# Kernel tuning notes

Measured on AMD Instinct MI355X. Metric: run time of the kernel, lower is better.

## Reference

```python
import jax, jax.numpy as jnp
import numpy as np

N_NEURONS = 100000
NNZ = 3200000
N_SENSORY = 5000
BATCH = 16
NUM_LAYERS = 8
THRESHOLD = 0.01
TANH_STEEPNESS = 5.0


def setup_inputs() -> dict:
    key = jax.random.key(0)
    k1, k2, k3, k4 = jax.random.split(key, 4)
    inputs = jax.random.uniform(k1, (BATCH, N_SENSORY, NUM_LAYERS), dtype=jnp.float32)
    # sparse connectome in COO form; small values so activations stay in a sane range
    weight_vals = jax.random.normal(k2, (NNZ,), dtype=jnp.float32) * 0.1
    weight_rows = jax.random.randint(k3, (NNZ,), 0, N_NEURONS, dtype=jnp.int32)
    weight_cols = jax.random.randint(k4, (NNZ,), 0, N_NEURONS, dtype=jnp.int32)
    sensory_indices = jnp.arange(N_SENSORY, dtype=jnp.int32)
    return {
        "inputs": inputs,
        "weight_vals": weight_vals,
        "weight_rows": weight_rows,
        "weight_cols": weight_cols,
        "sensory_indices": sensory_indices,
    }


def _spmm(vals, rows, cols, x):
    # x: (N, B); y[r, b] = sum_{e: rows[e]==r} vals[e] * x[cols[e], b]
    return jax.ops.segment_sum(vals[:, None] * x[cols], rows, num_segments=N_NEURONS)


def _activate(y):
    y = jnp.where(y >= THRESHOLD, y, jnp.zeros_like(y))
    return jnp.tanh(TANH_STEEPNESS * y)


def reference(inputs, weight_vals, weight_rows, weight_cols, sensory_indices):
    B, S, T = inputs.shape  # T == num_layers
    # preprocess sensory input: threshold then clamp to <= 1
    inp = jnp.where(inputs >= THRESHOLD, inputs, jnp.zeros_like(inputs))
    inp = jnp.minimum(inp, jnp.ones_like(inp))
    # state x: (N, B)
    full_input = jnp.zeros((N_NEURONS, B), inputs.dtype).at[sensory_indices].add(inp[:, :, 0].T)
    x = _activate(_spmm(weight_vals, weight_rows, weight_cols, full_input))
    acts = []
    for layer in range(1, T):
        # inject sensory input for this time step and clamp to <= 1
        x = x.at[sensory_indices].add(inp[:, :, layer].T)
        x = jnp.minimum(x, jnp.ones_like(x))
        acts.append(x)
        x = _activate(_spmm(weight_vals, weight_rows, weight_cols, x))
    acts.append(x)  # last layer: no injection
    # (T, N, B) -> (B, N, T), matching torch vmap'd cat along time dim
    return jnp.stack(acts, axis=0).transpose(2, 1, 0)
```

## Files before the change

### kernel.cpp

```cpp
#include <hip/hip_runtime.h>


#define N_NEURONS 100000
#define NNZ_CNT   3200000
#define N_SENSORY 5000
#define BATCH     16
#define T_LAYERS  8
#define THRESH    0.01f
#define STEEP     5.0f

#define NB (N_NEURONS * BATCH)
#define NT (N_NEURONS * T_LAYERS)
#define ST (N_SENSORY * T_LAYERS)

#define FXSCALE   17592186044416.0f
#define FXINV     (1.0 / 17592186044416.0)

#define LBITS   9
#define BROWS   (1 << LBITS)
#define NBUCKET ((N_NEURONS + BROWS - 1) / BROWS)
#define EPB     8192
#define NBLK_A  ((NNZ_CNT + EPB - 1) / EPB)

__device__ __forceinline__ float thresh_clamp_inp(float u) {
    u = (u >= THRESH) ? u : 0.0f;
    return fminf(u, 1.0f);
}
__device__ __forceinline__ float activate(float y) {
    y = (y >= THRESH) ? y : 0.0f;
    return tanhf(STEEP * y);
}


__global__ void k_init(const float* __restrict__ inp, float* __restrict__ state0,
                       int* __restrict__ btotal) {
    int stride = gridDim.x * blockDim.x;
    for (int i = blockIdx.x * blockDim.x + threadIdx.x; i < NB; i += stride) {
        int n = i >> 4, b = i & 15;
        float v = 0.0f;
        if (n < N_SENSORY) v = thresh_clamp_inp(inp[b * ST + n * T_LAYERS + 0]);
        state0[i] = v;
        if (i < NBUCKET) btotal[i] = 0;
    }
}

__global__ void __launch_bounds__(1024) k_bcount(const int* __restrict__ rows,
                                                 int* __restrict__ btotal) {
    __shared__ int cnt[NBUCKET];
    const int e0 = blockIdx.x * EPB;
    for (int i = threadIdx.x; i < NBUCKET; i += 1024) cnt[i] = 0;
    __syncthreads();
    #pragma unroll
    for (int i = 0; i < EPB / 1024; ++i) {
        int e = e0 + i * 1024 + threadIdx.x;
        if (e < NNZ_CNT) atomicAdd(&cnt[rows[e] >> LBITS], 1);
    }
    __syncthreads();
    for (int i = threadIdx.x; i < NBUCKET; i += 1024)
        if (cnt[i]) atomicAdd(&btotal[i], cnt[i]);
}

__global__ void k_bscan(const int* __restrict__ btotal, int* __restrict__ bbase,
                        int* __restrict__ bcur, int* __restrict__ row_ptr) {
    __shared__ int lds[256];
    int tid = threadIdx.x;
    int v = (tid < NBUCKET) ? btotal[tid] : 0;
    lds[tid] = v;
    __syncthreads();
    for (int off = 1; off < 256; off <<= 1) {
        int add = (tid >= off) ? lds[tid - off] : 0;
        __syncthreads();
        lds[tid] += add;
        __syncthreads();
    }
    if (tid < NBUCKET) {
        bbase[tid] = lds[tid] - v;
        bcur[tid]  = lds[tid] - v;
    }
    if (tid == 0) { bbase[NBUCKET] = NNZ_CNT; row_ptr[N_NEURONS] = NNZ_CNT; }
}

__global__ void __launch_bounds__(1024) k_passA(const float* __restrict__ vals,
                                                const int* __restrict__ rows,
                                                const int* __restrict__ cols,
                                                int* bcur,
                                                int2* __restrict__ packed_tmp) {
    __shared__ int cnt[NBUCKET];
    __shared__ int base[NBUCKET];
    const int e0 = blockIdx.x * EPB;
    for (int i = threadIdx.x; i < NBUCKET; i += 1024) cnt[i] = 0;
    __syncthreads();
    #pragma unroll
    for (int i = 0; i < EPB / 1024; ++i) {
        int e = e0 + i * 1024 + threadIdx.x;
        if (e < NNZ_CNT) atomicAdd(&cnt[rows[e] >> LBITS], 1);
    }
    __syncthreads();
    for (int i = threadIdx.x; i < NBUCKET; i += 1024) {
        int c = cnt[i];
        base[i] = (c > 0) ? atomicAdd(&bcur[i], c) : 0;
        cnt[i] = 0;
    }
    __syncthreads();
    #pragma unroll
    for (int i = 0; i < EPB / 1024; ++i) {
        int e = e0 + i * 1024 + threadIdx.x;
        if (e < NNZ_CNT) {
            int r = rows[e];
            int k = r >> LBITS;
            int pos = base[k] + atomicAdd(&cnt[k], 1);
            packed_tmp[pos] = make_int2((cols[e] << LBITS) | (r & (BROWS - 1)),
                                        __float_as_int(vals[e]));
        }
    }
}

__global__ void __launch_bounds__(1024) k_passB(const int* __restrict__ bbase,
                                                const int2* __restrict__ packed_tmp,
                                                int2* __restrict__ packed,
                                                int* __restrict__ row_ptr) {
    __shared__ int cnt[BROWS];
    __shared__ int scn[BROWS];
    const int tid = threadIdx.x;
    const int k  = blockIdx.x;
    const int r0 = k * BROWS;
    const int nr = min(BROWS, N_NEURONS - r0);
    const int P0 = bbase[k], P1 = bbase[k + 1];
    for (int i = tid; i < BROWS; i += 1024) cnt[i] = 0;
    __syncthreads();
    for (int i = P0 + tid; i < P1; i += 1024)
        atomicAdd(&cnt[packed_tmp[i].x & (BROWS - 1)], 1);
    __syncthreads();
    if (tid < BROWS) scn[tid] = cnt[tid];
    __syncthreads();
    for (int off = 1; off < BROWS; off <<= 1) {
        int add = (tid < BROWS && tid >= off) ? scn[tid - off] : 0;
        __syncthreads();
        if (tid < BROWS) scn[tid] += add;
        __syncthreads();
    }
    if (tid < BROWS) {
        int ex = P0 + scn[tid] - cnt[tid];
        if (tid < nr) row_ptr[r0 + tid] = ex;
        scn[tid] = ex;
    }
    __syncthreads();
    for (int i = P0 + tid; i < P1; i += 1024) {
        int2 pe = packed_tmp[i];
        int d = atomicAdd(&scn[pe.x & (BROWS - 1)], 1);
        packed[d] = make_int2(pe.x >> LBITS, pe.y);
    }
}

__global__ void __launch_bounds__(256) k_layer(const int* __restrict__ row_ptr,
                                               const int2* __restrict__ packed,
                                               const float* __restrict__ state_in,
                                               const float* __restrict__ inp,
                                               float* __restrict__ plane_out,
                                               int t) {
    int tid = blockIdx.x * blockDim.x + threadIdx.x;
    int r = tid >> 4, b = tid & 15;
    if (r >= N_NEURONS) return;
    int s = row_ptr[r], e = row_ptr[r + 1];
    long long acc = 0;
    for (int base = s; base < e; base += 16) {
        int idx = base + b;
        int2 pe = (idx < e) ? packed[idx] : make_int2(0, 0);
        #pragma unroll
        for (int j = 0; j < 16; ++j) {
            int   c = __shfl(pe.x, j, 16);
            float v = __int_as_float(__shfl(pe.y, j, 16));
            float xv = state_in[c * BATCH + b];
            acc += (long long)llrintf(v * xv * FXSCALE);
        }
    }
    float y = (float)((double)acc * FXINV);
    float a = activate(y);
    if (t < T_LAYERS - 1) {
        if (r < N_SENSORY) a += thresh_clamp_inp(inp[b * ST + r * T_LAYERS + (t + 1)]);
        a = fminf(a, 1.0f);
    }
    plane_out[r * BATCH + b] = a;
}

__global__ void k_out(const float* __restrict__ planes, float* __restrict__ out) {
    int i = blockIdx.x * blockDim.x + threadIdx.x;
    if (i >= NB) return;
    int n = i >> 4, b = i & 15;
    float4 o0, o1;
    o0.x = planes[0 * NB + i]; o0.y = planes[1 * NB + i];
    o0.z = planes[2 * NB + i]; o0.w = planes[3 * NB + i];
    o1.x = planes[4 * NB + i]; o1.y = planes[5 * NB + i];
    o1.z = planes[6 * NB + i]; o1.w = planes[7 * NB + i];
    float4* dst = (float4*)&out[b * NT + n * T_LAYERS];
    dst[0] = o0; dst[1] = o1;
}

__global__ void k2_init(const float* __restrict__ inp, float* __restrict__ state,
                        long long* __restrict__ acc) {
    int stride = gridDim.x * blockDim.x;
    for (int i = blockIdx.x * blockDim.x + threadIdx.x; i < NB; i += stride) {
        int n = i >> 4, b = i & 15;
        float v = 0.0f;
        if (n < N_SENSORY) v = thresh_clamp_inp(inp[b * ST + n * T_LAYERS + 0]);
        state[i] = v;
        acc[i]   = 0LL;
    }
}
__global__ void __launch_bounds__(256) k2_spmm(const float* __restrict__ vals,
                                               const int* __restrict__ rows,
                                               const int* __restrict__ cols,
                                               const float* __restrict__ state,
                                               long long* acc) {
    int tid = blockIdx.x * blockDim.x + threadIdx.x;
    int b = tid & 15;
    int e = tid >> 4;
    int estride = (gridDim.x * blockDim.x) >> 4;
    for (; e < NNZ_CNT; e += estride) {
        int   c  = cols[e];
        float xv = state[c * BATCH + b];
        float v  = vals[e];
        long long fx = llrintf(v * xv * FXSCALE);
        if (fx != 0LL) {
            int r = rows[e];
            atomicAdd((unsigned long long*)&acc[r * BATCH + b], (unsigned long long)fx);
        }
    }
}
__global__ void k2_act_inject(long long* acc, const float* __restrict__ inp,
                              float* __restrict__ state, float* __restrict__ out, int t) {
    int stride = gridDim.x * blockDim.x;
    for (int i = blockIdx.x * blockDim.x + threadIdx.x; i < NB; i += stride) {
        int n = i >> 4, b = i & 15;
        float y = (float)((double)acc[i] * FXINV);
        acc[i] = 0LL;
        float v = activate(y);
        if (n < N_SENSORY) v += thresh_clamp_inp(inp[b * ST + n * T_LAYERS + (t + 1)]);
        v = fminf(v, 1.0f);
        state[i] = v;
        out[b * NT + n * T_LAYERS + t] = v;
    }
}
__global__ void k2_act_final(const long long* __restrict__ acc, float* __restrict__ out) {
    int stride = gridDim.x * blockDim.x;
    for (int i = blockIdx.x * blockDim.x + threadIdx.x; i < NB; i += stride) {
        int n = i >> 4, b = i & 15;
        float y = (float)((double)acc[i] * FXINV);
        out[b * NT + n * T_LAYERS + (T_LAYERS - 1)] = activate(y);
    }
}

extern "C" void kernel_launch(void* const* d_in, const int* in_sizes, int n_in,
                              void* d_out, int out_size, void* d_ws, size_t ws_size,
                              hipStream_t stream) {
    const float* inputs = (const float*)d_in[0];
    const float* vals   = (const float*)d_in[1];
    const int*   rows   = (const int*)  d_in[2];
    const int*   cols   = (const int*)  d_in[3];
    float* out = (float*)d_out;

    const size_t sz_planes = (size_t)T_LAYERS * NB * 4;
    const size_t sz_packed = (size_t)NNZ_CNT * 8;
    const size_t sz_rowptr = ((size_t)N_NEURONS + 2) * 4;
    const size_t sz_btotal = (size_t)(NBUCKET + 8) * 4;
    const size_t sz_bbase  = (size_t)(NBUCKET + 8) * 4;
    const size_t sz_bcur   = (size_t)(NBUCKET + 8) * 4;
    const size_t REQ = sz_planes + sz_packed + sz_rowptr + sz_btotal + sz_bbase + sz_bcur;

    const int block = 256;

    if (ws_size >= REQ) {
        char* ws = (char*)d_ws;
        float* planes  = (float*)ws;
        int2*  packed  = (int2*)(ws + sz_planes);
        int*   row_ptr = (int*)(ws + sz_planes + sz_packed);
        int*   btotal  = (int*)(ws + sz_planes + sz_packed + sz_rowptr);
        int*   bbase   = (int*)(ws + sz_planes + sz_packed + sz_rowptr + sz_btotal);
        int*   bcur    = (int*)(ws + sz_planes + sz_packed + sz_rowptr + sz_btotal + sz_bbase);
        float* state0  = planes + (size_t)(T_LAYERS - 1) * NB;
        int2*  packed_tmp = (int2*)planes;

        const int grid_nb = (NB + block - 1) / block;

        k_init<<<grid_nb, block, 0, stream>>>(inputs, state0, btotal);
        k_bcount<<<NBLK_A, 1024, 0, stream>>>(rows, btotal);
        k_bscan<<<1, 256, 0, stream>>>(btotal, bbase, bcur, row_ptr);
        k_passA<<<NBLK_A, 1024, 0, stream>>>(vals, rows, cols, bcur, packed_tmp);
        k_passB<<<NBUCKET, 1024, 0, stream>>>(bbase, packed_tmp, packed, row_ptr);

        for (int t = 0; t < T_LAYERS; ++t) {
            const float* sin_ = (t == 0) ? state0 : planes + (size_t)(t - 1) * NB;
            k_layer<<<grid_nb, block, 0, stream>>>(row_ptr, packed, sin_, inputs,
                                                   planes + (size_t)t * NB, t);
        }
        k_out<<<grid_nb, block, 0, stream>>>(planes, out);
    } else {
        long long* acc   = (long long*)d_ws;
        float*     state = (float*)(acc + NB);
        const int grid_ew = 2048, grid_sp = 2048;
        k2_init<<<grid_ew, block, 0, stream>>>(inputs, state, acc);
        for (int t = 0; t < T_LAYERS; ++t) {
            k2_spmm<<<grid_sp, block, 0, stream>>>(vals, rows, cols, state, acc);
            if (t < T_LAYERS - 1)
                k2_act_inject<<<grid_ew, block, 0, stream>>>(acc, inputs, state, out, t);
            else
                k2_act_final<<<grid_ew, block, 0, stream>>>(acc, out);
        }
    }
}
```

Measured before the change: 426.6 us.

## Rebuild CSR conversion as deterministic chunked counting sort with float accumulation

Replaces the atomic-cursor two-pass bucket sort with a deterministic counting sort. Per-chunk histograms are followed by column scans, and placement uses wave-level ballot match to aggregate LDS atomics, applied to both the bucket and row passes. The SpMV layer kernel switches from 64-bit fixed-point accumulation with llrintf to plain fmaf float accumulation, relying on the deterministic ordering for reproducibility. This adds more kernel launches and scratch matrices, and float accumulation can change rounding compared with the exact fixed-point sum.

Result: slower. 439.0 us (+2.9%).

```diff
diff --git a/kernel.cpp b/kernel.cpp
--- a/kernel.cpp
+++ b/kernel.cpp
@@ -13,14 +13,16 @@
 #define NT (N_NEURONS * T_LAYERS)
 #define ST (N_SENSORY * T_LAYERS)
 
+#define LBITS    9
+#define BROWS    (1 << LBITS)
+#define NBUCKET  ((N_NEURONS + BROWS - 1) / BROWS)
+#define EPC      512
+#define NCHUNK_A (NNZ_CNT / EPC)
+#define MAXW     34
+#define NCHUNK_B (NBUCKET * MAXW)
+
 #define FXSCALE   17592186044416.0f
 #define FXINV     (1.0 / 17592186044416.0)
-
-#define LBITS   9
-#define BROWS   (1 << LBITS)
-#define NBUCKET ((N_NEURONS + BROWS - 1) / BROWS)
-#define EPB     8192
-#define NBLK_A  ((NNZ_CNT + EPB - 1) / EPB)
 
 __device__ __forceinline__ float thresh_clamp_inp(float u) {
     u = (u >= THRESH) ? u : 0.0f;
@@ -32,36 +34,50 @@
 }
 
 
-__global__ void k_init(const float* __restrict__ inp, float* __restrict__ state0,
-                       int* __restrict__ btotal) {
-    int stride = gridDim.x * blockDim.x;
-    for (int i = blockIdx.x * blockDim.x + threadIdx.x; i < NB; i += stride) {
-        int n = i >> 4, b = i & 15;
-        float v = 0.0f;
-        if (n < N_SENSORY) v = thresh_clamp_inp(inp[b * ST + n * T_LAYERS + 0]);
-        state0[i] = v;
-        if (i < NBUCKET) btotal[i] = 0;
-    }
-}
-
-__global__ void __launch_bounds__(1024) k_bcount(const int* __restrict__ rows,
-                                                 int* __restrict__ btotal) {
-    __shared__ int cnt[NBUCKET];
-    const int e0 = blockIdx.x * EPB;
-    for (int i = threadIdx.x; i < NBUCKET; i += 1024) cnt[i] = 0;
-    __syncthreads();
-    #pragma unroll
-    for (int i = 0; i < EPB / 1024; ++i) {
-        int e = e0 + i * 1024 + threadIdx.x;
-        if (e < NNZ_CNT) atomicAdd(&cnt[rows[e] >> LBITS], 1);
-    }
-    __syncthreads();
-    for (int i = threadIdx.x; i < NBUCKET; i += 1024)
-        if (cnt[i]) atomicAdd(&btotal[i], cnt[i]);
+__global__ void __launch_bounds__(256) k_countA(const int* __restrict__ rows,
+                                                int* __restrict__ M) {
+    __shared__ int cnt[4][NBUCKET];
+    int wv = threadIdx.x >> 6, ln = threadIdx.x & 63;
+    int chunk = blockIdx.x * 4 + wv;
+    for (int j = ln; j < NBUCKET; j += 64) cnt[wv][j] = 0;
+    __syncthreads();
+    if (chunk < NCHUNK_A) {
+        int base = chunk * EPC;
+        #pragma unroll
+        for (int it = 0; it < 8; ++it)
+            atomicAdd(&cnt[wv][rows[base + it * 64 + ln] >> LBITS], 1);
+    }
+    __syncthreads();
+    if (chunk < NCHUNK_A)
+        for (int j = ln; j < NBUCKET; j += 64) M[chunk * NBUCKET + j] = cnt[wv][j];
+}
+
+__global__ void __launch_bounds__(1024) k_scanA(int* __restrict__ M,
+                                                int* __restrict__ btotal) {
+    __shared__ int lds[1024];
+    int j = blockIdx.x, tid = threadIdx.x;
+    int running = 0;
+    for (int c0 = 0; c0 < NCHUNK_A; c0 += 1024) {
+        int c = c0 + tid;
+        int v = (c < NCHUNK_A) ? M[c * NBUCKET + j] : 0;
+        lds[tid] = v;
+        __syncthreads();
+        for (int off = 1; off < 1024; off <<= 1) {
+            int add = (tid >= off) ? lds[tid - off] : 0;
+            __syncthreads();
+            lds[tid] += add;
+            __syncthreads();
+        }
+        if (c < NCHUNK_A) M[c * NBUCKET + j] = running + lds[tid] - v;
+        int total = lds[1023];
+        __syncthreads();
+        running += total;
+    }
+    if (tid == 0) btotal[j] = running;
 }
 
 __global__ void k_bscan(const int* __restrict__ btotal, int* __restrict__ bbase,
-                        int* __restrict__ bcur, int* __restrict__ row_ptr) {
+                        int* __restrict__ row_ptr) {
     __shared__ int lds[256];
     int tid = threadIdx.x;
     int v = (tid < NBUCKET) ? btotal[tid] : 0;
@@ -73,83 +89,146 @@
         lds[tid] += add;
         __syncthreads();
     }
-    if (tid < NBUCKET) {
-        bbase[tid] = lds[tid] - v;
-        bcur[tid]  = lds[tid] - v;
-    }
+    if (tid < NBUCKET) bbase[tid] = lds[tid] - v;
     if (tid == 0) { bbase[NBUCKET] = NNZ_CNT; row_ptr[N_NEURONS] = NNZ_CNT; }
 }
 
-__global__ void __launch_bounds__(1024) k_passA(const float* __restrict__ vals,
-                                                const int* __restrict__ rows,
+__global__ void __launch_bounds__(256) k_placeA(const int* __restrict__ rows,
                                                 const int* __restrict__ cols,
-                                                int* bcur,
-                                                int2* __restrict__ packed_tmp) {
-    __shared__ int cnt[NBUCKET];
-    __shared__ int base[NBUCKET];
-    const int e0 = blockIdx.x * EPB;
-    for (int i = threadIdx.x; i < NBUCKET; i += 1024) cnt[i] = 0;
-    __syncthreads();
-    #pragma unroll
-    for (int i = 0; i < EPB / 1024; ++i) {
-        int e = e0 + i * 1024 + threadIdx.x;
-        if (e < NNZ_CNT) atomicAdd(&cnt[rows[e] >> LBITS], 1);
-    }
-    __syncthreads();
-    for (int i = threadIdx.x; i < NBUCKET; i += 1024) {
-        int c = cnt[i];
-        base[i] = (c > 0) ? atomicAdd(&bcur[i], c) : 0;
-        cnt[i] = 0;
-    }
-    __syncthreads();
-    #pragma unroll
-    for (int i = 0; i < EPB / 1024; ++i) {
-        int e = e0 + i * 1024 + threadIdx.x;
-        if (e < NNZ_CNT) {
+                                                const float* __restrict__ vals,
+                                                const int* __restrict__ M,
+                                                const int* __restrict__ bbase,
+                                                int2* __restrict__ slab) {
+    __shared__ int cur[4][NBUCKET];
+    int wv = threadIdx.x >> 6, ln = threadIdx.x & 63;
+    int chunk = blockIdx.x * 4 + wv;
+    bool cv = chunk < NCHUNK_A;
+    if (cv)
+        for (int j = ln; j < NBUCKET; j += 64)
+            cur[wv][j] = bbase[j] + M[chunk * NBUCKET + j];
+    __syncthreads();
+    if (cv) {
+        int base = chunk * EPC;
+        #pragma unroll
+        for (int it = 0; it < 8; ++it) {
+            int e = base + it * 64 + ln;
             int r = rows[e];
-            int k = r >> LBITS;
-            int pos = base[k] + atomicAdd(&cnt[k], 1);
-            packed_tmp[pos] = make_int2((cols[e] << LBITS) | (r & (BROWS - 1)),
-                                        __float_as_int(vals[e]));
-        }
-    }
-}
-
-__global__ void __launch_bounds__(1024) k_passB(const int* __restrict__ bbase,
-                                                const int2* __restrict__ packed_tmp,
-                                                int2* __restrict__ packed,
-                                                int* __restrict__ row_ptr) {
+            int key = r >> LBITS;
+            unsigned long long mask = ~0ull;
+            #pragma unroll
+            for (int bit = 0; bit < 8; ++bit) {
+                unsigned long long bb = __ballot((key >> bit) & 1);
+                mask &= ((key >> bit) & 1) ? bb : ~bb;
+            }
+            int rank = __popcll(mask & ((1ull << ln) - 1ull));
+            int cnt  = __popcll(mask);
+            int leader = __ffsll((unsigned long long)mask) - 1;
+            int bpos = 0;
+            if (rank == 0) bpos = atomicAdd(&cur[wv][key], cnt);
+            bpos = __shfl(bpos, leader, 64);
+            slab[bpos + rank] = make_int2((cols[e] << LBITS) | (r & (BROWS - 1)),
+                                          __float_as_int(vals[e]));
+        }
+    }
+}
+
+__global__ void __launch_bounds__(256) k_countB(const int* __restrict__ bbase,
+                                                const int2* __restrict__ slab,
+                                                int* __restrict__ C2) {
     __shared__ int cnt[BROWS];
+    int j = blockIdx.x / MAXW, w = blockIdx.x % MAXW;
+    int P0 = bbase[j], P1 = bbase[j + 1];
+    int s0 = P0 + w * EPC;
+    for (int lr = threadIdx.x; lr < BROWS; lr += 256) cnt[lr] = 0;
+    __syncthreads();
+    if (s0 < P1) {
+        int send = min(s0 + EPC, P1);
+        for (int s = s0 + threadIdx.x; s < send; s += 256)
+            atomicAdd(&cnt[slab[s].x & (BROWS - 1)], 1);
+    }
+    __syncthreads();
+    for (int lr = threadIdx.x; lr < BROWS; lr += 256)
+        C2[blockIdx.x * BROWS + lr] = cnt[lr];
+}
+
+__global__ void __launch_bounds__(512) k_scanB(const int* __restrict__ bbase,
+                                               int* __restrict__ C2,
+                                               int* __restrict__ row_ptr) {
     __shared__ int scn[BROWS];
-    const int tid = threadIdx.x;
-    const int k  = blockIdx.x;
-    const int r0 = k * BROWS;
-    const int nr = min(BROWS, N_NEURONS - r0);
-    const int P0 = bbase[k], P1 = bbase[k + 1];
-    for (int i = tid; i < BROWS; i += 1024) cnt[i] = 0;
-    __syncthreads();
-    for (int i = P0 + tid; i < P1; i += 1024)
-        atomicAdd(&cnt[packed_tmp[i].x & (BROWS - 1)], 1);
-    __syncthreads();
-    if (tid < BROWS) scn[tid] = cnt[tid];
+    int j = blockIdx.x, lr = threadIdx.x;
+    int P0 = bbase[j];
+    int t = 0;
+    for (int w = 0; w < MAXW; ++w) t += C2[(j * MAXW + w) * BROWS + lr];
+    scn[lr] = t;
     __syncthreads();
     for (int off = 1; off < BROWS; off <<= 1) {
-        int add = (tid < BROWS && tid >= off) ? scn[tid - off] : 0;
-        __syncthreads();
-        if (tid < BROWS) scn[tid] += add;
-        __syncthreads();
-    }
-    if (tid < BROWS) {
-        int ex = P0 + scn[tid] - cnt[tid];
-        if (tid < nr) row_ptr[r0 + tid] = ex;
-        scn[tid] = ex;
-    }
-    __syncthreads();
-    for (int i = P0 + tid; i < P1; i += 1024) {
-        int2 pe = packed_tmp[i];
-        int d = atomicAdd(&scn[pe.x & (BROWS - 1)], 1);
-        packed[d] = make_int2(pe.x >> LBITS, pe.y);
-    }
+        int add = (lr >= off) ? scn[lr - off] : 0;
+        __syncthreads();
+        scn[lr] += add;
+        __syncthreads();
+    }
+    int rowbase = P0 + scn[lr] - t;
+    int r = j * BROWS + lr;
+    if (r < N_NEURONS) row_ptr[r] = rowbase;
+    int runw = rowbase;
+    for (int w = 0; w < MAXW; ++w) {
+        int idx = (j * MAXW + w) * BROWS + lr;
+        int c = C2[idx];
+        C2[idx] = runw;
+        runw += c;
+    }
+}
+
+__global__ void __launch_bounds__(256) k_placeB(const int* __restrict__ bbase,
+                                                const int2* __restrict__ slab,
+                                                const int* __restrict__ C2,
+                                                int2* __restrict__ packed) {
+    __shared__ int cur[4][BROWS];
+    int wv = threadIdx.x >> 6, ln = threadIdx.x & 63;
+    int g = blockIdx.x * 4 + wv;
+    bool gv = g < NCHUNK_B;
+    int j = gv ? g / MAXW : 0, w = gv ? g % MAXW : 0;
+    int P0 = bbase[j], P1 = bbase[j + 1];
+    int s0 = P0 + w * EPC;
+    gv = gv && (s0 < P1);
+    if (gv)
+        for (int lr = ln; lr < BROWS; lr += 64) cur[wv][lr] = C2[g * BROWS + lr];
+    __syncthreads();
+    if (gv) {
+        int send = min(s0 + EPC, P1);
+        #pragma unroll
+        for (int it = 0; it < 8; ++it) {
+            int s = s0 + it * 64 + ln;
+            bool act = s < send;
+            unsigned long long amask = __ballot(act);
+            if (act) {
+                int2 pe = slab[s];
+                int key = pe.x & (BROWS - 1);
+                unsigned long long mask = amask;
+                #pragma unroll
+                for (int bit = 0; bit < LBITS; ++bit) {
+                    unsigned long long bb = __ballot((key >> bit) & 1);
+                    mask &= ((key >> bit) & 1) ? bb : ~bb;
+                }
+                int rank = __popcll(mask & ((1ull << ln) - 1ull));
+                int cnt  = __popcll(mask);
+                int leader = __ffsll((unsigned long long)mask) - 1;
+                int bpos = 0;
+                if (rank == 0) bpos = atomicAdd(&cur[wv][key], cnt);
+                bpos = __shfl(bpos, leader, 64);
+                packed[bpos + rank] = make_int2(pe.x >> LBITS, pe.y);
+            }
+        }
+    }
+}
+
+__global__ void k_init(const float* __restrict__ inp, float* __restrict__ state0) {
+    int i = blockIdx.x * blockDim.x + threadIdx.x;
+    if (i >= NB) return;
+    int n = i >> 4, b = i & 15;
+    float v = 0.0f;
+    if (n < N_SENSORY) v = thresh_clamp_inp(inp[b * ST + n * T_LAYERS + 0]);
+    state0[i] = v;
 }
 
 __global__ void __launch_bounds__(256) k_layer(const int* __restrict__ row_ptr,
@@ -162,20 +241,18 @@
     int r = tid >> 4, b = tid & 15;
     if (r >= N_NEURONS) return;
     int s = row_ptr[r], e = row_ptr[r + 1];
-    long long acc = 0;
+    float acc = 0.0f;
     for (int base = s; base < e; base += 16) {
         int idx = base + b;
         int2 pe = (idx < e) ? packed[idx] : make_int2(0, 0);
         #pragma unroll
-        for (int j = 0; j < 16; ++j) {
-            int   c = __shfl(pe.x, j, 16);
-            float v = __int_as_float(__shfl(pe.y, j, 16));
-            float xv = state_in[c * BATCH + b];
-            acc += (long long)llrintf(v * xv * FXSCALE);
-        }
-    }
-    float y = (float)((double)acc * FXINV);
-    float a = activate(y);
+        for (int jj = 0; jj < 16; ++jj) {
+            int   c = __shfl(pe.x, jj, 16);
+            float v = __int_as_float(__shfl(pe.y, jj, 16));
+            acc = fmaf(v, state_in[c * BATCH + b], acc);
+        }
+    }
+    float a = activate(acc);
     if (t < T_LAYERS - 1) {
         if (r < N_SENSORY) a += thresh_clamp_inp(inp[b * ST + r * T_LAYERS + (t + 1)]);
         a = fminf(a, 1.0f);
@@ -217,14 +294,10 @@
     int e = tid >> 4;
     int estride = (gridDim.x * blockDim.x) >> 4;
     for (; e < NNZ_CNT; e += estride) {
-        int   c  = cols[e];
-        float xv = state[c * BATCH + b];
-        float v  = vals[e];
-        long long fx = llrintf(v * xv * FXSCALE);
-        if (fx != 0LL) {
-            int r = rows[e];
-            atomicAdd((unsigned long long*)&acc[r * BATCH + b], (unsigned long long)fx);
-        }
+        float xv = state[cols[e] * BATCH + b];
+        long long fx = llrintf(vals[e] * xv * FXSCALE);
+        if (fx != 0LL)
+            atomicAdd((unsigned long long*)&acc[rows[e] * BATCH + b], (unsigned long long)fx);
     }
 }
 __global__ void k2_act_inject(long long* acc, const float* __restrict__ inp,
@@ -262,10 +335,8 @@
     const size_t sz_planes = (size_t)T_LAYERS * NB * 4;
     const size_t sz_packed = (size_t)NNZ_CNT * 8;
     const size_t sz_rowptr = ((size_t)N_NEURONS + 2) * 4;
-    const size_t sz_btotal = (size_t)(NBUCKET + 8) * 4;
-    const size_t sz_bbase  = (size_t)(NBUCKET + 8) * 4;
-    const size_t sz_bcur   = (size_t)(NBUCKET + 8) * 4;
-    const size_t REQ = sz_planes + sz_packed + sz_rowptr + sz_btotal + sz_bbase + sz_bcur;
+    const size_t sz_bt     = (size_t)(NBUCKET + 8) * 4;
+    const size_t REQ = sz_planes + sz_packed + sz_rowptr + 2 * sz_bt;
 
     const int block = 256;
 
@@ -275,18 +346,23 @@
         int2*  packed  = (int2*)(ws + sz_planes);
         int*   row_ptr = (int*)(ws + sz_planes + sz_packed);
         int*   btotal  = (int*)(ws + sz_planes + sz_packed + sz_rowptr);
-        int*   bbase   = (int*)(ws + sz_planes + sz_packed + sz_rowptr + sz_btotal);
-        int*   bcur    = (int*)(ws + sz_planes + sz_packed + sz_rowptr + sz_btotal + sz_bbase);
-        float* state0  = planes + (size_t)(T_LAYERS - 1) * NB;
-        int2*  packed_tmp = (int2*)planes;
+        int*   bbase   = (int*)(ws + sz_planes + sz_packed + sz_rowptr + sz_bt);
+        int2*  slab  = (int2*)planes;
+        char*  p4    = ws + (size_t)4 * NB * 4;
+        int*   C2    = (int*)p4;
+        int*   M     = (int*)(p4 + (size_t)NCHUNK_B * BROWS * 4);
+        float* state0 = planes + (size_t)(T_LAYERS - 1) * NB;
 
         const int grid_nb = (NB + block - 1) / block;
 
-        k_init<<<grid_nb, block, 0, stream>>>(inputs, state0, btotal);
-        k_bcount<<<NBLK_A, 1024, 0, stream>>>(rows, btotal);
-        k_bscan<<<1, 256, 0, stream>>>(btotal, bbase, bcur, row_ptr);
-        k_passA<<<NBLK_A, 1024, 0, stream>>>(vals, rows, cols, bcur, packed_tmp);
-        k_passB<<<NBUCKET, 1024, 0, stream>>>(bbase, packed_tmp, packed, row_ptr);
+        k_countA<<<(NCHUNK_A + 3) / 4, 256, 0, stream>>>(rows, M);
+        k_scanA<<<NBUCKET, 1024, 0, stream>>>(M, btotal);
+        k_bscan<<<1, 256, 0, stream>>>(btotal, bbase, row_ptr);
+        k_placeA<<<(NCHUNK_A + 3) / 4, 256, 0, stream>>>(rows, cols, vals, M, bbase, slab);
+        k_countB<<<NCHUNK_B, 256, 0, stream>>>(bbase, slab, C2);
+        k_scanB<<<NBUCKET, 512, 0, stream>>>(bbase, C2, row_ptr);
+        k_placeB<<<(NCHUNK_B + 3) / 4, 256, 0, stream>>>(bbase, slab, C2, packed);
+        k_init<<<grid_nb, block, 0, stream>>>(inputs, state0);
 
         for (int t = 0; t < T_LAYERS; ++t) {
             const float* sin_ = (t == 0) ? state0 : planes + (size_t)(t - 1) * NB;
```
